# Kernel optimization log

Hardware: AMD Instinct MI355X
Metric: run time of the kernel (lower is better)

The kernel has to match this reference:

```python
import jax, jax.numpy as jnp
import numpy as np

B, H, L, V = 128, 1024, 60, 50257


def setup_inputs() -> dict:
    key = jax.random.key(0)
    ks = jax.random.split(key, 14)
    s = 0.02
    f32 = jnp.float32
    return {
        "input": jax.random.randint(ks[0], (B,), 0, V),
        "hidden": jax.random.normal(ks[1], (1, B, H), f32),
        "encoder_outputs": jax.random.normal(ks[2], (B, L, H), f32),
        # learned parameters
        "emb": (jax.random.normal(ks[3], (V, H), f32) * s),
        "attn_W": (jax.random.normal(ks[4], (L, 2 * H), f32) * s),
        "attn_b": jnp.zeros((L,), f32),
        "comb_W": (jax.random.normal(ks[5], (H, 2 * H), f32) * s),
        "comb_b": jnp.zeros((H,), f32),
        "W_ih": (jax.random.normal(ks[6], (3 * H, H), f32) * s),
        "W_hh": (jax.random.normal(ks[7], (3 * H, H), f32) * s),
        "b_ih": jnp.zeros((3 * H,), f32),
        "b_hh": jnp.zeros((3 * H,), f32),
        "out_W": (jax.random.normal(ks[8], (V, H), f32) * s),
        "out_b": jnp.zeros((V,), f32),
    }


def reference(input, hidden, encoder_outputs, emb, attn_W, attn_b,
              comb_W, comb_b, W_ih, W_hh, b_ih, b_hh, out_W, out_b):
    # embedding lookup (dropout is identity in eval mode)
    embedded = emb[input]                      # [B, H]
    h = hidden[0]                              # [B, H]

    # Bahdanau-style attention over fixed max_length positions
    attn_logits = jnp.concatenate([embedded, h], axis=1) @ attn_W.T + attn_b  # [B, L]
    attn_weights = jax.nn.softmax(attn_logits, axis=1)                        # [B, L]
    attn_applied = jnp.einsum('bl,blh->bh', attn_weights, encoder_outputs)    # [B, H]

    # combine + relu
    x = jnp.concatenate([embedded, attn_applied], axis=1) @ comb_W.T + comb_b  # [B, H]
    x = jax.nn.relu(x)

    # single GRU step (PyTorch gate order: r, z, n)
    gi = x @ W_ih.T + b_ih                     # [B, 3H]
    gh = h @ W_hh.T + b_hh                     # [B, 3H]
    i_r, i_z, i_n = jnp.split(gi, 3, axis=1)
    h_r, h_z, h_n = jnp.split(gh, 3, axis=1)
    r = jax.nn.sigmoid(i_r + h_r)
    z = jax.nn.sigmoid(i_z + h_z)
    n = jnp.tanh(i_n + r * h_n)
    h_new = (1.0 - z) * n + z * h              # [B, H]

    # output projection + log_softmax over vocab
    logp = jax.nn.log_softmax(h_new @ out_W.T + out_b, axis=1)  # [B, V]
    return logp, h_new[None], attn_weights
```

## Files before the change

### kernel.cpp

```cpp
#include <hip/hip_runtime.h>
#include <hip/hip_bf16.h>

#define B_ 128
#define H_ 1024
#define L_ 60
#define V_ 50257

typedef __attribute__((ext_vector_type(8))) short bf16x8;
typedef __attribute__((ext_vector_type(4))) float f32x4;

__device__ __forceinline__ unsigned short f2bf(float f) {
  union { __hip_bfloat16 h; unsigned short u; } v;
  v.h = __float2bfloat16(f);
  return v.u;
}

__device__ __forceinline__ bf16x8 cvt8(float4 a, float4 b) {
  union { bf16x8 v; __hip_bfloat16 h[8]; } u;
  u.h[0] = __float2bfloat16(a.x); u.h[1] = __float2bfloat16(a.y);
  u.h[2] = __float2bfloat16(a.z); u.h[3] = __float2bfloat16(a.w);
  u.h[4] = __float2bfloat16(b.x); u.h[5] = __float2bfloat16(b.y);
  u.h[6] = __float2bfloat16(b.z); u.h[7] = __float2bfloat16(b.w);
  return u.v;
}

__device__ __forceinline__ void gl_lds16(const void* g, void* l) {
  __builtin_amdgcn_global_load_lds(
      (const __attribute__((address_space(1))) unsigned int*)g,
      (__attribute__((address_space(3))) unsigned int*)l, 16, 0, 0);
}

#define SBAR()   __builtin_amdgcn_s_barrier()
#define SCHED0() __builtin_amdgcn_sched_barrier(0)
__device__ __forceinline__ void vwait4() { asm volatile("s_waitcnt vmcnt(4)" ::: "memory"); }
__device__ __forceinline__ void vwait0() { asm volatile("s_waitcnt vmcnt(0)" ::: "memory"); }

__device__ __forceinline__ size_t packIdx(int b, int k) {
  int s = k >> 5;
  int bm = b >> 4;
  int lane = (b & 15) | (((k >> 3) & 3) << 4);
  return ((size_t)((s * 8 + bm) * 64 + lane) << 3) | (size_t)(k & 7);
}

__global__ __launch_bounds__(256) void k_embh(
    const int* __restrict__ input, const float* __restrict__ hidden,
    const float* __restrict__ emb, unsigned short* __restrict__ aXa,
    unsigned short* __restrict__ aH)
{
  int idx = blockIdx.x * 256 + threadIdx.x;
  int b = idx >> 10, j = idx & (H_ - 1);
  float e = emb[(size_t)input[b] * H_ + j];
  float h = hidden[idx];
  size_t p = packIdx(b, j);
  aXa[p] = f2bf(e);
  aH[p]  = f2bf(h);
}

__global__ __launch_bounds__(256) void k_alog(
    const int* __restrict__ input, const float* __restrict__ hidden,
    const float* __restrict__ emb, const float* __restrict__ attn_W,
    const float* __restrict__ attn_b, float* __restrict__ lbuf)
{
  int t = threadIdx.x, wv = t >> 6, lane = t & 63;
  int task = blockIdx.x * 4 + wv;
  int b = task / L_, l = task - b * L_;
  const float* erow = emb + (size_t)input[b] * H_;
  const float* hrow = hidden + (size_t)b * H_;
  const float* wr = attn_W + (size_t)l * (2 * H_);
  float acc = 0.f;
  #pragma unroll 4
  for (int i = 0; i < 16; ++i) {
    int m = lane + i * 64;
    acc += erow[m] * wr[m] + hrow[m] * wr[H_ + m];
  }
  #pragma unroll
  for (int off = 32; off; off >>= 1) acc += __shfl_xor(acc, off);
  if (lane == 0) lbuf[b * 64 + l] = acc + attn_b[l];
}

__global__ __launch_bounds__(256) void k_asm(
    const float* __restrict__ lbuf, float* __restrict__ attnw,
    float* __restrict__ wbuf)
{
  int t = threadIdx.x, wv = t >> 6, lane = t & 63;
  int b = blockIdx.x * 4 + wv;
  float v = (lane < L_) ? lbuf[b * 64 + lane] : -1e30f;
  float m = v;
  #pragma unroll
  for (int off = 32; off; off >>= 1) m = fmaxf(m, __shfl_xor(m, off));
  float e = (lane < L_) ? __expf(v - m) : 0.f;
  float s = e;
  #pragma unroll
  for (int off = 32; off; off >>= 1) s += __shfl_xor(s, off);
  float w = e / s;
  if (lane < L_) { attnw[b * L_ + lane] = w; wbuf[b * 64 + lane] = w; }
}

__global__ __launch_bounds__(256) void k_app(
    const float* __restrict__ enc, const float* __restrict__ wbuf,
    unsigned short* __restrict__ aXa)
{
  __shared__ float sWt[64];
  int b = blockIdx.x, q = blockIdx.y, t = threadIdx.x;
  if (t < L_) sWt[t] = wbuf[b * 64 + t];
  __syncthreads();
  int col = q * 256 + t;
  const float* eb = enc + (size_t)b * L_ * H_ + col;
  float acc = 0.f;
  #pragma unroll 4
  for (int l = 0; l < L_; ++l) acc += sWt[l] * eb[(size_t)l * H_];
  aXa[packIdx(b, H_ + col)] = f2bf(acc);
}

__global__ __launch_bounds__(256, 6) void k_gemm(
    const unsigned short* __restrict__ Apk, const unsigned short* __restrict__ Apk2,
    const float* __restrict__ Wt, const float* __restrict__ Wt2,
    const float* __restrict__ bias, float* __restrict__ Cdir,
    float* __restrict__ Cpart, float* __restrict__ Cpart2,
    float* __restrict__ pms, int K, int N, int nchunks, int halfY, int nblkx)
{
  __shared__ __align__(16) float bufW0[64 * 32];
  __shared__ __align__(16) float bufW1[64 * 32];
  int t = threadIdx.x, wv = t >> 6, lane = t & 63;
  int y = blockIdx.y;
  const unsigned short* A = Apk;
  const float* W = Wt;
  float* CP = Cpart;
  int sidx = y;
  if (halfY && y >= halfY) { A = Apk2; W = Wt2; CP = Cpart2; sidx = y - halfY; }
  int chunk0 = sidx * nchunks;
  int n0 = blockIdx.x * 64;
  int bm0 = wv * 2;
  int srow8 = lane >> 3;
  int sch = lane & 7;
  int g = lane >> 4;

  f32x4 acc[2][4];
  #pragma unroll
  for (int i = 0; i < 2; ++i)
    #pragma unroll
    for (int j = 0; j < 4; ++j) acc[i][j] = (f32x4){0.f, 0.f, 0.f, 0.f};

  auto SW = [&](int kc, float* buf) {
    #pragma unroll
    for (int i = 0; i < 2; ++i) {
      int r = wv * 16 + i * 8 + srow8;
      int gcol = n0 + r; gcol = (gcol < N) ? gcol : (N - 1);
      int c = sch ^ (r & 7);
      const float* src = W + (size_t)gcol * K + (size_t)kc * 32 + c * 4;
      gl_lds16(src, buf + (wv * 16 + i * 8) * 32);
    }
  };
  const bf16x8* apg = (const bf16x8*)A;
  auto LA = [&](int kc, bf16x8& x0, bf16x8& x1) {
    x0 = apg[((size_t)kc * 8 + bm0) * 64 + lane];
    x1 = apg[((size_t)kc * 8 + bm0 + 1) * 64 + lane];
  };
  auto COMP = [&](const float* bw, bf16x8 a0, bf16x8 a1) {
    #pragma unroll
    for (int nc = 0; nc < 4; ++nc) {
      int rr = nc * 16 + (lane & 15);
      int c0 = (g * 2) ^ (rr & 7);
      int c1 = (g * 2 + 1) ^ (rr & 7);
      float4 w0 = *(const float4*)&bw[rr * 32 + c0 * 4];
      float4 w1 = *(const float4*)&bw[rr * 32 + c1 * 4];
      bf16x8 bfr = cvt8(w0, w1);
      acc[0][nc] = __builtin_amdgcn_mfma_f32_16x16x32_bf16(a0, bfr, acc[0][nc], 0, 0, 0);
      acc[1][nc] = __builtin_amdgcn_mfma_f32_16x16x32_bf16(a1, bfr, acc[1][nc], 0, 0, 0);
    }
  };

  bf16x8 aA0, aA1, aB0, aB1;
  SW(chunk0, bufW0);     LA(chunk0, aA0, aA1);
  SW(chunk0 + 1, bufW1); LA(chunk0 + 1, aB0, aB1);
  vwait4(); SCHED0(); SBAR();

  for (int kk = 0; kk < nchunks; kk += 2) {
    COMP(bufW0, aA0, aA1);
    SCHED0(); SBAR();
    if (kk + 2 < nchunks) { SW(chunk0 + kk + 2, bufW0); LA(chunk0 + kk + 2, aA0, aA1); vwait4(); }
    else vwait0();
    SCHED0(); SBAR();
    COMP(bufW1, aB0, aB1);
    if (kk + 2 < nchunks) {
      SCHED0(); SBAR();
      if (kk + 3 < nchunks) { SW(chunk0 + kk + 3, bufW1); LA(chunk0 + kk + 3, aB0, aB1); vwait4(); }
      else vwait0();
      SCHED0(); SBAR();
    }
  }

  int cols[4]; float bv[4];
  #pragma unroll
  for (int nc = 0; nc < 4; ++nc) {
    int c = n0 + nc * 16 + (lane & 15);
    cols[nc] = c;
    bv[nc] = (bias && c < N) ? bias[c] : 0.f;
  }
  int rb = (lane >> 4) * 4;
  if (CP) {
    float* dst = CP + (size_t)sidx * B_ * N;
    #pragma unroll
    for (int bm = 0; bm < 2; ++bm)
      #pragma unroll
      for (int r = 0; r < 4; ++r) {
        int row = (bm0 + bm) * 16 + rb + r;
        #pragma unroll
        for (int nc = 0; nc < 4; ++nc)
          if (cols[nc] < N) dst[(size_t)row * N + cols[nc]] = acc[bm][nc][r];
      }
  } else {
    #pragma unroll
    for (int bm = 0; bm < 2; ++bm)
      #pragma unroll
      for (int r = 0; r < 4; ++r) {
        int row = (bm0 + bm) * 16 + rb + r;
        #pragma unroll
        for (int nc = 0; nc < 4; ++nc)
          if (cols[nc] < N) Cdir[(size_t)row * N + cols[nc]] = acc[bm][nc][r] + bv[nc];
      }
    if (pms) {
      #pragma unroll
      for (int bm = 0; bm < 2; ++bm)
        #pragma unroll
        for (int r = 0; r < 4; ++r) {
          int row = (bm0 + bm) * 16 + rb + r;
          float m = -1e30f;
          #pragma unroll
          for (int nc = 0; nc < 4; ++nc)
            if (cols[nc] < N) m = fmaxf(m, acc[bm][nc][r] + bv[nc]);
          #pragma unroll
          for (int off = 8; off; off >>= 1) m = fmaxf(m, __shfl_xor(m, off));
          float e = 0.f;
          #pragma unroll
          for (int nc = 0; nc < 4; ++nc)
            if (cols[nc] < N) e += __expf(acc[bm][nc][r] + bv[nc] - m);
          #pragma unroll
          for (int off = 8; off; off >>= 1) e += __shfl_xor(e, off);
          if ((lane & 15) == 0) {
            size_t o = ((size_t)row * nblkx + blockIdx.x) * 2;
            pms[o] = m; pms[o + 1] = e;
          }
        }
    }
  }
}

__global__ __launch_bounds__(256) void k_reduce_comb(
    const float* __restrict__ parts, const float* __restrict__ bias,
    unsigned short* __restrict__ aX)
{
  int idx = blockIdx.x * 256 + threadIdx.x;
  int b = idx >> 10, j = idx & (H_ - 1);
  float s = bias[j];
  #pragma unroll
  for (int p = 0; p < 16; ++p) s += parts[(size_t)p * B_ * H_ + idx];
  s = fmaxf(s, 0.f);
  aX[packIdx(b, j)] = f2bf(s);
}

__global__ __launch_bounds__(256) void k_gate(
    const float* __restrict__ giP, const float* __restrict__ ghP,
    const float* __restrict__ b_ih, const float* __restrict__ b_hh,
    const float* __restrict__ hidden, float* __restrict__ hnew,
    unsigned short* __restrict__ aHn)
{
  int idx = blockIdx.x * 256 + threadIdx.x;
  int b = idx >> 10, j = idx & (H_ - 1);
  size_t base = (size_t)b * 3 * H_;
  float ir = b_ih[j], iz = b_ih[H_ + j], in_ = b_ih[2 * H_ + j];
  float hr = b_hh[j], hz = b_hh[H_ + j], hn = b_hh[2 * H_ + j];
  #pragma unroll
  for (int p = 0; p < 4; ++p) {
    const float* gi = giP + (size_t)p * B_ * 3 * H_ + base;
    const float* gh = ghP + (size_t)p * B_ * 3 * H_ + base;
    ir += gi[j]; iz += gi[H_ + j]; in_ += gi[2 * H_ + j];
    hr += gh[j]; hz += gh[H_ + j]; hn += gh[2 * H_ + j];
  }
  float r = 1.f / (1.f + __expf(-(ir + hr)));
  float z = 1.f / (1.f + __expf(-(iz + hz)));
  float n = tanhf(in_ + r * hn);
  float h = hidden[idx];
  float hv = (1.f - z) * n + z * h;
  hnew[idx] = hv;
  aHn[packIdx(b, j)] = f2bf(hv);
}

#define SL_ 6283
__global__ __launch_bounds__(256) void k_lsub(
    float* __restrict__ logits, const float* __restrict__ pms, int nblk)
{
  __shared__ float sm[4], ss[4], sc;
  int b = blockIdx.x, sl = blockIdx.y, t = threadIdx.x;
  float M = -1e30f, S = 0.f;
  for (int i = t; i < nblk; i += 256) {
    float m = pms[((size_t)b * nblk + i) * 2];
    float s = pms[((size_t)b * nblk + i) * 2 + 1];
    float nm = fmaxf(M, m);
    S = S * __expf(M - nm) + s * __expf(m - nm);
    M = nm;
  }
  #pragma unroll
  for (int off = 32; off; off >>= 1) {
    float m2 = __shfl_xor(M, off), s2 = __shfl_xor(S, off);
    float nm = fmaxf(M, m2);
    S = S * __expf(M - nm) + s2 * __expf(m2 - nm);
    M = nm;
  }
  if ((t & 63) == 0) { sm[t >> 6] = M; ss[t >> 6] = S; }
  __syncthreads();
  if (t == 0) {
    float Mf = sm[0], Sf = ss[0];
    #pragma unroll
    for (int i = 1; i < 4; ++i) {
      float nm = fmaxf(Mf, sm[i]);
      Sf = Sf * __expf(Mf - nm) + ss[i] * __expf(sm[i] - nm);
      Mf = nm;
    }
    sc = Mf + logf(Sf);
  }
  __syncthreads();
  float c = sc;
  int v0 = sl * SL_;
  int v1 = v0 + SL_; if (v1 > V_) v1 = V_;
  float* row = logits + (size_t)b * V_;
  for (int v = v0 + t; v < v1; v += 256) row[v] -= c;
}

extern "C" void kernel_launch(void* const* d_in, const int* in_sizes, int n_in,
                              void* d_out, int out_size, void* d_ws, size_t ws_size,
                              hipStream_t stream)
{
  const int*   input  = (const int*)d_in[0];
  const float* hidden = (const float*)d_in[1];
  const float* enc    = (const float*)d_in[2];
  const float* emb    = (const float*)d_in[3];
  const float* attn_W = (const float*)d_in[4];
  const float* attn_b = (const float*)d_in[5];
  const float* comb_W = (const float*)d_in[6];
  const float* comb_b = (const float*)d_in[7];
  const float* W_ih   = (const float*)d_in[8];
  const float* W_hh   = (const float*)d_in[9];
  const float* b_ih   = (const float*)d_in[10];
  const float* b_hh   = (const float*)d_in[11];
  const float* out_W  = (const float*)d_in[12];
  const float* out_b  = (const float*)d_in[13];

  float* out    = (float*)d_out;
  float* logits = out;
  float* hnew   = out + (size_t)B_ * V_;
  float* attnw  = hnew + (size_t)B_ * H_;

  const int NBLK = (V_ + 63) / 64;
  char* ws = (char*)d_ws;
  unsigned short* aXa = (unsigned short*)(ws);
  unsigned short* aH  = (unsigned short*)(ws + 524288);
  unsigned short* aX  = (unsigned short*)(ws + 786432);
  unsigned short* aHn = (unsigned short*)(ws + 1048576);
  float* wbuf  = (float*)(ws + 1310720);
  float* lbuf  = (float*)(ws + 1343488);
  float* pms   = (float*)(ws + 1376256);
  float* combP = (float*)(ws + 2185216);
  float* giP   = (float*)(ws + 2185216);
  float* ghP   = (float*)(ws + 2185216 + 6291456);

  k_embh<<<512, 256, 0, stream>>>(input, hidden, emb, aXa, aH);
  k_alog<<<(B_ * L_) / 4, 256, 0, stream>>>(input, hidden, emb, attn_W, attn_b, lbuf);
  k_asm<<<B_ / 4, 256, 0, stream>>>(lbuf, attnw, wbuf);
  k_app<<<dim3(B_, 4), 256, 0, stream>>>(enc, wbuf, aXa);
  k_gemm<<<dim3(16, 16), 256, 0, stream>>>(aXa, nullptr, comb_W, nullptr, nullptr,
                                           nullptr, combP, nullptr, nullptr,
                                           2 * H_, H_, 4, 0, 0);
  k_reduce_comb<<<(B_ * H_) / 256, 256, 0, stream>>>(combP, comb_b, aX);
  k_gemm<<<dim3(48, 8), 256, 0, stream>>>(aX, aH, W_ih, W_hh, nullptr,
                                          nullptr, giP, ghP, nullptr,
                                          H_, 3 * H_, 8, 4, 0);
  k_gate<<<(B_ * H_) / 256, 256, 0, stream>>>(giP, ghP, b_ih, b_hh, hidden, hnew, aHn);
  k_gemm<<<dim3(NBLK, 1), 256, 0, stream>>>(aHn, nullptr, out_W, nullptr, out_b,
                                            logits, nullptr, nullptr, pms,
                                            H_, V_, 32, 0, NBLK);
  k_lsub<<<dim3(B_, 8), 256, 0, stream>>>(logits, pms, NBLK);
}
```

Before: 135.1 us.

## Fuse front-end attention kernels and retile GEMM warps to 4x2 MFMA blocks

The embedding/hidden pack and attention-logit kernels are merged into one launch, and the attention softmax is folded into the attention-apply kernel, removing two launches and the wbuf round trip. The GEMM warp tiling changes from 2 row-blocks x 4 column-blocks to 4 row-blocks x 2 column-blocks per warp. Each warp now loads four A fragments and converts fewer B fragments from LDS, cutting redundant fp32-to-bf16 conversion and LDS reads. In exchange there are more A registers (launch bound lowered to 5), per-half-block partial max/sum entries in pms, and a relocated workspace layout.

Measured after the change: 130.2 us. 3.6% less time.

```diff
diff --git a/kernel.cpp b/kernel.cpp
--- a/kernel.cpp
+++ b/kernel.cpp
@@ -32,7 +32,7 @@
 
 #define SBAR()   __builtin_amdgcn_s_barrier()
 #define SCHED0() __builtin_amdgcn_sched_barrier(0)
-__device__ __forceinline__ void vwait4() { asm volatile("s_waitcnt vmcnt(4)" ::: "memory"); }
+__device__ __forceinline__ void vwait6() { asm volatile("s_waitcnt vmcnt(6)" ::: "memory"); }
 __device__ __forceinline__ void vwait0() { asm volatile("s_waitcnt vmcnt(0)" ::: "memory"); }
 
 __device__ __forceinline__ size_t packIdx(int b, int k) {
@@ -42,67 +42,59 @@
   return ((size_t)((s * 8 + bm) * 64 + lane) << 3) | (size_t)(k & 7);
 }
 
-__global__ __launch_bounds__(256) void k_embh(
-    const int* __restrict__ input, const float* __restrict__ hidden,
-    const float* __restrict__ emb, unsigned short* __restrict__ aXa,
-    unsigned short* __restrict__ aH)
-{
-  int idx = blockIdx.x * 256 + threadIdx.x;
-  int b = idx >> 10, j = idx & (H_ - 1);
-  float e = emb[(size_t)input[b] * H_ + j];
-  float h = hidden[idx];
-  size_t p = packIdx(b, j);
-  aXa[p] = f2bf(e);
-  aH[p]  = f2bf(h);
-}
-
-__global__ __launch_bounds__(256) void k_alog(
+__global__ __launch_bounds__(256) void k_front(
     const int* __restrict__ input, const float* __restrict__ hidden,
     const float* __restrict__ emb, const float* __restrict__ attn_W,
-    const float* __restrict__ attn_b, float* __restrict__ lbuf)
-{
-  int t = threadIdx.x, wv = t >> 6, lane = t & 63;
-  int task = blockIdx.x * 4 + wv;
-  int b = task / L_, l = task - b * L_;
-  const float* erow = emb + (size_t)input[b] * H_;
-  const float* hrow = hidden + (size_t)b * H_;
-  const float* wr = attn_W + (size_t)l * (2 * H_);
-  float acc = 0.f;
-  #pragma unroll 4
-  for (int i = 0; i < 16; ++i) {
-    int m = lane + i * 64;
-    acc += erow[m] * wr[m] + hrow[m] * wr[H_ + m];
-  }
-  #pragma unroll
-  for (int off = 32; off; off >>= 1) acc += __shfl_xor(acc, off);
-  if (lane == 0) lbuf[b * 64 + l] = acc + attn_b[l];
-}
-
-__global__ __launch_bounds__(256) void k_asm(
-    const float* __restrict__ lbuf, float* __restrict__ attnw,
-    float* __restrict__ wbuf)
-{
-  int t = threadIdx.x, wv = t >> 6, lane = t & 63;
-  int b = blockIdx.x * 4 + wv;
-  float v = (lane < L_) ? lbuf[b * 64 + lane] : -1e30f;
-  float m = v;
-  #pragma unroll
-  for (int off = 32; off; off >>= 1) m = fmaxf(m, __shfl_xor(m, off));
-  float e = (lane < L_) ? __expf(v - m) : 0.f;
-  float s = e;
-  #pragma unroll
-  for (int off = 32; off; off >>= 1) s += __shfl_xor(s, off);
-  float w = e / s;
-  if (lane < L_) { attnw[b * L_ + lane] = w; wbuf[b * 64 + lane] = w; }
-}
-
-__global__ __launch_bounds__(256) void k_app(
-    const float* __restrict__ enc, const float* __restrict__ wbuf,
-    unsigned short* __restrict__ aXa)
+    const float* __restrict__ attn_b, unsigned short* __restrict__ aXa,
+    unsigned short* __restrict__ aH, float* __restrict__ lbuf)
+{
+  int bx = blockIdx.x;
+  if (bx < 512) {
+    int idx = bx * 256 + threadIdx.x;
+    int b = idx >> 10, j = idx & (H_ - 1);
+    float e = emb[(size_t)input[b] * H_ + j];
+    float h = hidden[idx];
+    size_t p = packIdx(b, j);
+    aXa[p] = f2bf(e);
+    aH[p]  = f2bf(h);
+  } else {
+    int t = threadIdx.x, wv = t >> 6, lane = t & 63;
+    int task = (bx - 512) * 4 + wv;
+    int b = task / L_, l = task - b * L_;
+    const float* erow = emb + (size_t)input[b] * H_;
+    const float* hrow = hidden + (size_t)b * H_;
+    const float* wr = attn_W + (size_t)l * (2 * H_);
+    float acc = 0.f;
+    #pragma unroll 4
+    for (int i = 0; i < 16; ++i) {
+      int m = lane + i * 64;
+      acc += erow[m] * wr[m] + hrow[m] * wr[H_ + m];
+    }
+    #pragma unroll
+    for (int off = 32; off; off >>= 1) acc += __shfl_xor(acc, off);
+    if (lane == 0) lbuf[b * 64 + l] = acc + attn_b[l];
+  }
+}
+
+__global__ __launch_bounds__(256) void k_appsm(
+    const float* __restrict__ enc, const float* __restrict__ lbuf,
+    float* __restrict__ attnw, unsigned short* __restrict__ aXa)
 {
   __shared__ float sWt[64];
   int b = blockIdx.x, q = blockIdx.y, t = threadIdx.x;
-  if (t < L_) sWt[t] = wbuf[b * 64 + t];
+  if (t < 64) {
+    float v = (t < L_) ? lbuf[b * 64 + t] : -1e30f;
+    float m = v;
+    #pragma unroll
+    for (int off = 32; off; off >>= 1) m = fmaxf(m, __shfl_xor(m, off));
+    float e = (t < L_) ? __expf(v - m) : 0.f;
+    float s = e;
+    #pragma unroll
+    for (int off = 32; off; off >>= 1) s += __shfl_xor(s, off);
+    float w = e / s;
+    sWt[t] = w;
+    if (q == 0 && t < L_) attnw[b * L_ + t] = w;
+  }
   __syncthreads();
   int col = q * 256 + t;
   const float* eb = enc + (size_t)b * L_ * H_ + col;
@@ -112,7 +104,7 @@
   aXa[packIdx(b, H_ + col)] = f2bf(acc);
 }
 
-__global__ __launch_bounds__(256, 6) void k_gemm(
+__global__ __launch_bounds__(256, 5) void k_gemm(
     const unsigned short* __restrict__ Apk, const unsigned short* __restrict__ Apk2,
     const float* __restrict__ Wt, const float* __restrict__ Wt2,
     const float* __restrict__ bias, float* __restrict__ Cdir,
@@ -130,16 +122,17 @@
   if (halfY && y >= halfY) { A = Apk2; W = Wt2; CP = Cpart2; sidx = y - halfY; }
   int chunk0 = sidx * nchunks;
   int n0 = blockIdx.x * 64;
-  int bm0 = wv * 2;
+  int ch = wv & 1;
+  int bm0 = (wv >> 1) * 4;
   int srow8 = lane >> 3;
   int sch = lane & 7;
   int g = lane >> 4;
 
-  f32x4 acc[2][4];
-  #pragma unroll
-  for (int i = 0; i < 2; ++i)
-    #pragma unroll
-    for (int j = 0; j < 4; ++j) acc[i][j] = (f32x4){0.f, 0.f, 0.f, 0.f};
+  f32x4 acc[4][2];
+  #pragma unroll
+  for (int i = 0; i < 4; ++i)
+    #pragma unroll
+    for (int j = 0; j < 2; ++j) acc[i][j] = (f32x4){0.f, 0.f, 0.f, 0.f};
 
   auto SW = [&](int kc, float* buf) {
     #pragma unroll
@@ -152,93 +145,95 @@
     }
   };
   const bf16x8* apg = (const bf16x8*)A;
-  auto LA = [&](int kc, bf16x8& x0, bf16x8& x1) {
-    x0 = apg[((size_t)kc * 8 + bm0) * 64 + lane];
-    x1 = apg[((size_t)kc * 8 + bm0 + 1) * 64 + lane];
+  auto LA = [&](int kc, bf16x8* x) {
+    #pragma unroll
+    for (int j = 0; j < 4; ++j)
+      x[j] = apg[((size_t)kc * 8 + bm0 + j) * 64 + lane];
   };
-  auto COMP = [&](const float* bw, bf16x8 a0, bf16x8 a1) {
-    #pragma unroll
-    for (int nc = 0; nc < 4; ++nc) {
-      int rr = nc * 16 + (lane & 15);
+  auto COMP = [&](const float* bw, const bf16x8* a) {
+    #pragma unroll
+    for (int nci = 0; nci < 2; ++nci) {
+      int rr = (ch * 2 + nci) * 16 + (lane & 15);
       int c0 = (g * 2) ^ (rr & 7);
       int c1 = (g * 2 + 1) ^ (rr & 7);
       float4 w0 = *(const float4*)&bw[rr * 32 + c0 * 4];
       float4 w1 = *(const float4*)&bw[rr * 32 + c1 * 4];
       bf16x8 bfr = cvt8(w0, w1);
-      acc[0][nc] = __builtin_amdgcn_mfma_f32_16x16x32_bf16(a0, bfr, acc[0][nc], 0, 0, 0);
-      acc[1][nc] = __builtin_amdgcn_mfma_f32_16x16x32_bf16(a1, bfr, acc[1][nc], 0, 0, 0);
+      #pragma unroll
+      for (int j = 0; j < 4; ++j)
+        acc[j][nci] = __builtin_amdgcn_mfma_f32_16x16x32_bf16(a[j], bfr, acc[j][nci], 0, 0, 0);
     }
   };
 
-  bf16x8 aA0, aA1, aB0, aB1;
-  SW(chunk0, bufW0);     LA(chunk0, aA0, aA1);
-  SW(chunk0 + 1, bufW1); LA(chunk0 + 1, aB0, aB1);
-  vwait4(); SCHED0(); SBAR();
+  bf16x8 aA[4], aB[4];
+  SW(chunk0, bufW0);     LA(chunk0, aA);
+  SW(chunk0 + 1, bufW1); LA(chunk0 + 1, aB);
+  vwait6(); SCHED0(); SBAR();
 
   for (int kk = 0; kk < nchunks; kk += 2) {
-    COMP(bufW0, aA0, aA1);
+    COMP(bufW0, aA);
     SCHED0(); SBAR();
-    if (kk + 2 < nchunks) { SW(chunk0 + kk + 2, bufW0); LA(chunk0 + kk + 2, aA0, aA1); vwait4(); }
+    if (kk + 2 < nchunks) { SW(chunk0 + kk + 2, bufW0); LA(chunk0 + kk + 2, aA); vwait6(); }
     else vwait0();
     SCHED0(); SBAR();
-    COMP(bufW1, aB0, aB1);
+    COMP(bufW1, aB);
     if (kk + 2 < nchunks) {
       SCHED0(); SBAR();
-      if (kk + 3 < nchunks) { SW(chunk0 + kk + 3, bufW1); LA(chunk0 + kk + 3, aB0, aB1); vwait4(); }
+      if (kk + 3 < nchunks) { SW(chunk0 + kk + 3, bufW1); LA(chunk0 + kk + 3, aB); vwait6(); }
       else vwait0();
       SCHED0(); SBAR();
     }
   }
 
-  int cols[4]; float bv[4];
-  #pragma unroll
-  for (int nc = 0; nc < 4; ++nc) {
-    int c = n0 + nc * 16 + (lane & 15);
-    cols[nc] = c;
-    bv[nc] = (bias && c < N) ? bias[c] : 0.f;
+  int cols[2]; float bv[2];
+  #pragma unroll
+  for (int nci = 0; nci < 2; ++nci) {
+    int c = n0 + (ch * 2 + nci) * 16 + (lane & 15);
+    cols[nci] = c;
+    bv[nci] = (bias && c < N) ? bias[c] : 0.f;
   }
   int rb = (lane >> 4) * 4;
   if (CP) {
     float* dst = CP + (size_t)sidx * B_ * N;
     #pragma unroll
-    for (int bm = 0; bm < 2; ++bm)
+    for (int bm = 0; bm < 4; ++bm)
       #pragma unroll
       for (int r = 0; r < 4; ++r) {
         int row = (bm0 + bm) * 16 + rb + r;
         #pragma unroll
-        for (int nc = 0; nc < 4; ++nc)
-          if (cols[nc] < N) dst[(size_t)row * N + cols[nc]] = acc[bm][nc][r];
+        for (int nci = 0; nci < 2; ++nci)
+          if (cols[nci] < N) dst[(size_t)row * N + cols[nci]] = acc[bm][nci][r];
       }
   } else {
     #pragma unroll
-    for (int bm = 0; bm < 2; ++bm)
+    for (int bm = 0; bm < 4; ++bm)
       #pragma unroll
       for (int r = 0; r < 4; ++r) {
         int row = (bm0 + bm) * 16 + rb + r;
         #pragma unroll
-        for (int nc = 0; nc < 4; ++nc)
-          if (cols[nc] < N) Cdir[(size_t)row * N + cols[nc]] = acc[bm][nc][r] + bv[nc];
+        for (int nci = 0; nci < 2; ++nci)
+          if (cols[nci] < N) Cdir[(size_t)row * N + cols[nci]] = acc[bm][nci][r] + bv[nci];
       }
     if (pms) {
       #pragma unroll
-      for (int bm = 0; bm < 2; ++bm)
+      for (int bm = 0; bm < 4; ++bm)
         #pragma unroll
         for (int r = 0; r < 4; ++r) {
           int row = (bm0 + bm) * 16 + rb + r;
           float m = -1e30f;
           #pragma unroll
-          for (int nc = 0; nc < 4; ++nc)
-            if (cols[nc] < N) m = fmaxf(m, acc[bm][nc][r] + bv[nc]);
+          for (int nci = 0; nci < 2; ++nci)
+            if (cols[nci] < N) m = fmaxf(m, acc[bm][nci][r] + bv[nci]);
           #pragma unroll
           for (int off = 8; off; off >>= 1) m = fmaxf(m, __shfl_xor(m, off));
           float e = 0.f;
           #pragma unroll
-          for (int nc = 0; nc < 4; ++nc)
-            if (cols[nc] < N) e += __expf(acc[bm][nc][r] + bv[nc] - m);
+          for (int nci = 0; nci < 2; ++nci)
+            if (cols[nci] < N) e += __expf(acc[bm][nci][r] + bv[nci] - m);
           #pragma unroll
           for (int off = 8; off; off >>= 1) e += __shfl_xor(e, off);
           if ((lane & 15) == 0) {
-            size_t o = ((size_t)row * nblkx + blockIdx.x) * 2;
+            size_t o = ((size_t)row * (2 * nblkx) + blockIdx.x * 2 + ch) * 2;
             pms[o] = m; pms[o + 1] = e;
           }
         }
@@ -288,14 +283,14 @@
 
 #define SL_ 6283
 __global__ __launch_bounds__(256) void k_lsub(
-    float* __restrict__ logits, const float* __restrict__ pms, int nblk)
+    float* __restrict__ logits, const float* __restrict__ pms, int nblk2)
 {
   __shared__ float sm[4], ss[4], sc;
   int b = blockIdx.x, sl = blockIdx.y, t = threadIdx.x;
   float M = -1e30f, S = 0.f;
-  for (int i = t; i < nblk; i += 256) {
-    float m = pms[((size_t)b * nblk + i) * 2];
-    float s = pms[((size_t)b * nblk + i) * 2 + 1];
+  for (int i = t; i < nblk2; i += 256) {
+    float m = pms[((size_t)b * nblk2 + i) * 2];
+    float s = pms[((size_t)b * nblk2 + i) * 2 + 1];
     float nm = fmaxf(M, m);
     S = S * __expf(M - nm) + s * __expf(m - nm);
     M = nm;
@@ -357,17 +352,15 @@
   unsigned short* aH  = (unsigned short*)(ws + 524288);
   unsigned short* aX  = (unsigned short*)(ws + 786432);
   unsigned short* aHn = (unsigned short*)(ws + 1048576);
-  float* wbuf  = (float*)(ws + 1310720);
-  float* lbuf  = (float*)(ws + 1343488);
-  float* pms   = (float*)(ws + 1376256);
-  float* combP = (float*)(ws + 2185216);
-  float* giP   = (float*)(ws + 2185216);
-  float* ghP   = (float*)(ws + 2185216 + 6291456);
-
-  k_embh<<<512, 256, 0, stream>>>(input, hidden, emb, aXa, aH);
-  k_alog<<<(B_ * L_) / 4, 256, 0, stream>>>(input, hidden, emb, attn_W, attn_b, lbuf);
-  k_asm<<<B_ / 4, 256, 0, stream>>>(lbuf, attnw, wbuf);
-  k_app<<<dim3(B_, 4), 256, 0, stream>>>(enc, wbuf, aXa);
+  float* lbuf  = (float*)(ws + 1310720);
+  float* pms   = (float*)(ws + 1343488);
+  float* combP = (float*)(ws + 4194304);
+  float* giP   = (float*)(ws + 4194304);
+  float* ghP   = (float*)(ws + 4194304 + 6291456);
+
+  k_front<<<512 + (B_ * L_) / 4, 256, 0, stream>>>(input, hidden, emb, attn_W, attn_b,
+                                                   aXa, aH, lbuf);
+  k_appsm<<<dim3(B_, 4), 256, 0, stream>>>(enc, lbuf, attnw, aXa);
   k_gemm<<<dim3(16, 16), 256, 0, stream>>>(aXa, nullptr, comb_W, nullptr, nullptr,
                                            nullptr, combP, nullptr, nullptr,
                                            2 * H_, H_, 4, 0, 0);
@@ -379,5 +372,5 @@
   k_gemm<<<dim3(NBLK, 1), 256, 0, stream>>>(aHn, nullptr, out_W, nullptr, out_b,
                                             logits, nullptr, nullptr, pms,
                                             H_, V_, 32, 0, NBLK);
-  k_lsub<<<dim3(B_, 8), 256, 0, stream>>>(logits, pms, NBLK);
-}
+  k_lsub<<<dim3(B_, 8), 256, 0, stream>>>(logits, pms, 2 * NBLK);
+}
```
